# Kernel tuning notes

Hardware: AMD Instinct MI355X
Metric: run time of the kernel (lower is better)

## Reference

```python
import jax, jax.numpy as jnp
import numpy as np

B, N, C, H = 2048, 15, 1024, 16
HS = C // H  # 64
SCALE = HS ** -0.5
EPS = 1e-5


def _ln(x, g, b):
    m = jnp.mean(x, axis=-1, keepdims=True)
    v = jnp.mean(jnp.square(x - m), axis=-1, keepdims=True)
    return (x - m) * jax.lax.rsqrt(v + EPS) * g + b


def setup_inputs() -> dict:
    key = jax.random.key(0)
    ks = jax.random.split(key, 20)
    s = lambda fan_in: 1.0 / np.sqrt(fan_in)
    inp = {
        "joint_feature": jax.random.normal(ks[0], (B, N, C), jnp.float32),
        "relation_feature": jax.random.normal(ks[1], (B, N, C), jnp.float32),
        # weights stored as [in, out] (transposed vs torch Linear)
        "W_Jqkv": jax.random.uniform(ks[2], (C, 3 * C), jnp.float32, -s(C), s(C)),
        "W_Iqk": jax.random.uniform(ks[3], (C, 3 * C), jnp.float32, -s(C), s(C)),
        "W_Iconv": jax.random.uniform(ks[4], (HS, 15), jnp.float32, -s(HS), s(HS)),
        "W_proj": jax.random.uniform(ks[5], (C, C), jnp.float32, -s(C), s(C)),
        "b_proj": jax.random.uniform(ks[6], (C,), jnp.float32, -s(C), s(C)),
        "g_attn1": jnp.ones((C,), jnp.float32),
        "b_attn1": jnp.zeros((C,), jnp.float32),
        "g_attn2": jnp.ones((C,), jnp.float32),
        "b_attn2": jnp.zeros((C,), jnp.float32),
        "g_joint": jnp.ones((C,), jnp.float32),
        "b_joint": jnp.zeros((C,), jnp.float32),
        "W_fc1": jax.random.uniform(ks[7], (C, C // 2), jnp.float32, -s(C), s(C)),
        "b_fc1": jax.random.uniform(ks[8], (C // 2,), jnp.float32, -s(C), s(C)),
        "W_fc2": jax.random.uniform(ks[9], (C // 2, C), jnp.float32, -s(C // 2), s(C // 2)),
        "b_fc2": jax.random.uniform(ks[10], (C,), jnp.float32, -s(C // 2), s(C // 2)),
    }
    return inp


def reference(joint_feature, relation_feature, W_Jqkv, W_Iqk, W_Iconv, W_proj, b_proj,
              g_attn1, b_attn1, g_attn2, b_attn2, g_joint, b_joint,
              W_fc1, b_fc1, W_fc2, b_fc2):
    # --- Attention_I on normalized streams ---
    xj = _ln(joint_feature, g_attn1, b_attn1)      # [B,N,C]
    xi = _ln(relation_feature, g_attn2, b_attn2)   # [B,N,C]

    Jqkv = (xj @ W_Jqkv).reshape(B, N, 3, H, HS).transpose(2, 0, 3, 1, 4)  # [3,B,H,N,HS]
    Jq, Jk, Jv = Jqkv[0], Jqkv[1], Jqkv[2]
    Iqkv = (xi @ W_Iqk).reshape(B, N, 3, H, HS).transpose(2, 0, 3, 1, 4)
    Iq, Ik, Iv = Iqkv[0], Iqkv[1], Iqkv[2]

    attn_J = jnp.einsum("bhqd,bhkd->bhqk", Jq, Jk)
    attn_I = jnp.einsum("bhqd,bhkd->bhqk", Iq, Ik)
    attn_lin = Iv @ W_Iconv                        # [B,H,N,15] == [B,H,N,N]
    attn = jax.nn.softmax((attn_J + attn_I + attn_lin) * SCALE, axis=-1)

    x = jnp.einsum("bhqk,bhkd->bhqd", attn, Jv)    # [B,H,N,HS]
    x = x.transpose(0, 2, 1, 3).reshape(B, N, C)
    x = x @ W_proj + b_proj

    joint = joint_feature + x

    # --- MLP (hidden = dim // 2) ---
    y = _ln(joint, g_joint, b_joint)
    y = jax.nn.gelu(y @ W_fc1 + b_fc1, approximate=False)
    y = y @ W_fc2 + b_fc2
    return joint + y
```

## Files before the change

### kernel.cpp

```cpp
#include <hip/hip_runtime.h>
#include <math.h>


typedef __attribute__((ext_vector_type(8))) short short8;
typedef __attribute__((ext_vector_type(8))) unsigned short ush8;
typedef __attribute__((ext_vector_type(4))) float fx4;

#define MROWS 30720

#define GLL16(g, l)                                                         \
    __builtin_amdgcn_global_load_lds(                                       \
        (const __attribute__((address_space(1))) unsigned int*)(g),         \
        (__attribute__((address_space(3))) unsigned int*)(l), 16, 0, 0)

__device__ inline unsigned short f2bf(float f) {
    unsigned int u = __float_as_uint(f);
    unsigned int r = (u + 0x7fffu + ((u >> 16) & 1u)) >> 16;
    return (unsigned short)r;
}
__device__ inline float bf2f(unsigned short s) {
    return __uint_as_float(((unsigned int)s) << 16);
}

__global__ __launch_bounds__(256) void transpose_w(const float* __restrict__ W,
                                                   unsigned short* __restrict__ Wt,
                                                   int K, int N) {
    __shared__ float tile[32][33];
    int bn = blockIdx.x * 32;
    int bk = blockIdx.y * 32;
    int tx = threadIdx.x & 31, ty = threadIdx.x >> 5;
    #pragma unroll
    for (int i = ty; i < 32; i += 8)
        tile[i][tx] = W[(size_t)(bk + i) * N + bn + tx];
    __syncthreads();
    #pragma unroll
    for (int i = ty; i < 32; i += 8)
        Wt[(size_t)(bn + i) * K + bk + tx] = f2bf(tile[tx][i]);
}

__global__ __launch_bounds__(256) void ln_dual(const float* __restrict__ xa,
                                               const float* __restrict__ ga,
                                               const float* __restrict__ bba,
                                               unsigned short* __restrict__ oa,
                                               const float* __restrict__ xb,
                                               const float* __restrict__ gb,
                                               const float* __restrict__ bbb,
                                               unsigned short* __restrict__ ob) {
    const float* x = blockIdx.y ? xb : xa;
    const float* g = blockIdx.y ? gb : ga;
    const float* bv = blockIdx.y ? bbb : bba;
    unsigned short* out = blockIdx.y ? ob : oa;

    int row = blockIdx.x;
    int t = threadIdx.x;
    const float4* xp = (const float4*)(x + (size_t)row * 1024);
    float4 v = xp[t];
    float s  = v.x + v.y + v.z + v.w;
    float ss = v.x * v.x + v.y * v.y + v.z * v.z + v.w * v.w;
    #pragma unroll
    for (int o = 32; o > 0; o >>= 1) { s += __shfl_down(s, o); ss += __shfl_down(ss, o); }
    __shared__ float ps[4], pss[4], stat[2];
    int wv = t >> 6, ln = t & 63;
    if (ln == 0) { ps[wv] = s; pss[wv] = ss; }
    __syncthreads();
    if (t == 0) {
        float S = ps[0] + ps[1] + ps[2] + ps[3];
        float SS = pss[0] + pss[1] + pss[2] + pss[3];
        float m = S * (1.0f / 1024.0f);
        float var = SS * (1.0f / 1024.0f) - m * m;
        stat[0] = m; stat[1] = rsqrtf(var + 1e-5f);
    }
    __syncthreads();
    float m = stat[0], r = stat[1];
    float4 gg = ((const float4*)g)[t];
    float4 bb = ((const float4*)bv)[t];
    ushort4 o;
    o.x = f2bf((v.x - m) * r * gg.x + bb.x);
    o.y = f2bf((v.y - m) * r * gg.y + bb.y);
    o.z = f2bf((v.z - m) * r * gg.z + bb.z);
    o.w = f2bf((v.w - m) * r * gg.w + bb.w);
    ((ushort4*)(out + (size_t)row * 1024))[t] = o;
}

template <int EPI, int K>
__global__ __launch_bounds__(256) void gemm_lds(const unsigned short* __restrict__ A,
                                                const unsigned short* __restrict__ Bt,
                                                const unsigned short* __restrict__ A2,
                                                const unsigned short* __restrict__ Bt2,
                                                const float* __restrict__ bias,
                                                const float* __restrict__ resid,
                                                float* __restrict__ outF,
                                                unsigned short* __restrict__ outB,
                                                unsigned short* __restrict__ outB2,
                                                int N) {
    if (EPI == 0 && blockIdx.z) { A = A2; Bt = Bt2; outB = outB2; }

    __shared__ __align__(16) char smem[32768];
    unsigned short* lA = (unsigned short*)smem;
    unsigned short* lB = (unsigned short*)(smem + 16384);

    const int tid = threadIdx.x;
    const int wave = tid >> 6, lane = tid & 63;
    const int rowf = lane & 15, quad = lane >> 4;

    int bx = blockIdx.x, by = blockIdx.y;
    if (gridDim.x <= 8) {
        int nwg = gridDim.x * gridDim.y;
        int lid = by * gridDim.x + bx;
        int q = nwg >> 3, r = nwg & 7;
        int xcd = lid & 7, pos = lid >> 3;
        int nl = (xcd < r ? xcd * (q + 1) : r * (q + 1) + (xcd - r) * q) + pos;
        bx = nl % gridDim.x;
        by = nl / gridDim.x;
    }

    const int m0 = by * 128;
    const int n0 = bx * 128;
    const int wm0 = (wave >> 1) * 64;
    const int wn0 = (wave & 1) * 64;

    const int srow = tid >> 2;
    const int skc  = (tid & 3) * 8;
    const unsigned short* gA0 = A  + (size_t)(m0 + srow) * K + skc;
    const unsigned short* gA1 = A  + (size_t)(m0 + srow + 64) * K + skc;
    const unsigned short* gB0 = Bt + (size_t)(n0 + srow) * K + skc;
    const unsigned short* gB1 = Bt + (size_t)(n0 + srow + 64) * K + skc;

    fx4 acc[4][4] = {};

    const int NT = K / 32;

    GLL16(gA0, lA + (size_t)tid * 8);
    GLL16(gA1, lA + (size_t)(tid + 256) * 8);
    GLL16(gB0, lB + (size_t)tid * 8);
    GLL16(gB1, lB + (size_t)(tid + 256) * 8);
    gA0 += 32; gA1 += 32; gB0 += 32; gB1 += 32;
    __syncthreads();

    #pragma unroll 2
    for (int t = 0; t < NT; ++t) {
        const int cur = t & 1, nxt = cur ^ 1;
        if (t + 1 < NT) {
            GLL16(gA0, lA + nxt * 4096 + (size_t)tid * 8);
            GLL16(gA1, lA + nxt * 4096 + (size_t)(tid + 256) * 8);
            GLL16(gB0, lB + nxt * 4096 + (size_t)tid * 8);
            GLL16(gB1, lB + nxt * 4096 + (size_t)(tid + 256) * 8);
            gA0 += 32; gA1 += 32; gB0 += 32; gB1 += 32;
        }
        const unsigned short* sA = lA + cur * 4096;
        const unsigned short* sB = lB + cur * 4096;
        short8 a[4], b[4];
        #pragma unroll
        for (int i = 0; i < 4; i++)
            a[i] = *(const short8*)(sA + (wm0 + 16 * i + rowf) * 32 + quad * 8);
        #pragma unroll
        for (int j = 0; j < 4; j++)
            b[j] = *(const short8*)(sB + (wn0 + 16 * j + rowf) * 32 + quad * 8);
        #pragma unroll
        for (int i = 0; i < 4; i++)
            #pragma unroll
            for (int j = 0; j < 4; j++)
                acc[i][j] = __builtin_amdgcn_mfma_f32_16x16x32_bf16(a[i], b[j], acc[i][j], 0, 0, 0);
        asm volatile("s_waitcnt vmcnt(0) lgkmcnt(0)\n\ts_barrier" ::: "memory");
    }

    float* st = (float*)smem + wave * 1280;
    const int rl  = lane >> 2;
    const int c0l = (lane & 3) * 16;
    const int colb = n0 + wn0 + c0l;

    #pragma unroll
    for (int i = 0; i < 4; i++) {
        #pragma unroll
        for (int j = 0; j < 4; j++)
            #pragma unroll
            for (int r = 0; r < 4; r++)
                st[(quad * 4 + r) * 80 + 16 * j + rowf] = acc[i][j][r];
        const int row = m0 + wm0 + 16 * i + rl;
        if (EPI == 1) {
            #pragma unroll
            for (int kk = 0; kk < 4; kk++) {
                float4 v  = *(const float4*)(st + rl * 80 + c0l + 4 * kk);
                float4 bb = *((const float4*)(bias + colb) + kk);
                float4 rr = *((const float4*)(resid + (size_t)row * N + colb) + kk);
                v.x += bb.x + rr.x; v.y += bb.y + rr.y;
                v.z += bb.z + rr.z; v.w += bb.w + rr.w;
                *((float4*)(outF + (size_t)row * N + colb) + kk) = v;
            }
        } else {
            #pragma unroll
            for (int h = 0; h < 2; h++) {
                float4 va = *(const float4*)(st + rl * 80 + c0l + 8 * h);
                float4 vb = *(const float4*)(st + rl * 80 + c0l + 8 * h + 4);
                float f[8] = {va.x, va.y, va.z, va.w, vb.x, vb.y, vb.z, vb.w};
                if (EPI == 2) {
                    float4 ba = *((const float4*)(bias + colb) + 2 * h);
                    float4 bc = *((const float4*)(bias + colb) + 2 * h + 1);
                    float bf[8] = {ba.x, ba.y, ba.z, ba.w, bc.x, bc.y, bc.z, bc.w};
                    #pragma unroll
                    for (int e = 0; e < 8; e++) {
                        float v = f[e] + bf[e];
                        f[e] = 0.5f * v * (1.0f + erff(v * 0.70710678118654752f));
                    }
                }
                ush8 o;
                #pragma unroll
                for (int e = 0; e < 8; e++) o[e] = f2bf(f[e]);
                *(ush8*)(outB + (size_t)row * N + colb + 8 * h) = o;
            }
        }
    }
}

__global__ __launch_bounds__(256) void attn_kernel(const unsigned short* __restrict__ Jqkv,
                                                   const unsigned short* __restrict__ Iqkv,
                                                   const float* __restrict__ Wc,
                                                   unsigned short* __restrict__ xout) {
    int b = blockIdx.x >> 4;
    int h = blockIdx.x & 15;
    __shared__ float J[3][15][65];
    __shared__ float I[3][15][65];
    __shared__ float W[64][17];
    __shared__ float P[15][16];

    const unsigned short* Jb = Jqkv + (size_t)b * 15 * 3072 + h * 64;
    const unsigned short* Ib = Iqkv + (size_t)b * 15 * 3072 + h * 64;

    for (int idx = threadIdx.x; idx < 360; idx += 256) {
        int n = idx / 24, rem = idx % 24;
        int r = rem >> 3, d0 = (rem & 7) * 8;
        short8 vj = *(const short8*)(Jb + (size_t)n * 3072 + r * 1024 + d0);
        short8 vi = *(const short8*)(Ib + (size_t)n * 3072 + r * 1024 + d0);
        #pragma unroll
        for (int e = 0; e < 8; e++) {
            J[r][n][d0 + e] = bf2f((unsigned short)vj[e]);
            I[r][n][d0 + e] = bf2f((unsigned short)vi[e]);
        }
    }
    for (int idx = threadIdx.x; idx < 64 * 15; idx += 256)
        W[idx / 15][idx % 15] = Wc[idx];
    __syncthreads();

    for (int idx = threadIdx.x; idx < 225; idx += 256) {
        int q = idx / 15, kk = idx % 15;
        float s = 0.0f;
        #pragma unroll 8
        for (int d = 0; d < 64; d++)
            s += J[0][q][d] * J[1][kk][d] + I[0][q][d] * I[1][kk][d] + I[2][q][d] * W[d][kk];
        P[q][kk] = s * 0.125f;
    }
    __syncthreads();

    if (threadIdx.x < 15) {
        int q = threadIdx.x;
        float mx = -1e30f;
        #pragma unroll
        for (int kk = 0; kk < 15; kk++) mx = fmaxf(mx, P[q][kk]);
        float e[15], sum = 0.0f;
        #pragma unroll
        for (int kk = 0; kk < 15; kk++) { e[kk] = __expf(P[q][kk] - mx); sum += e[kk]; }
        float inv = 1.0f / sum;
        #pragma unroll
        for (int kk = 0; kk < 15; kk++) P[q][kk] = e[kk] * inv;
    }
    __syncthreads();

    for (int idx = threadIdx.x; idx < 240; idx += 256) {
        int q = idx >> 4, d0 = (idx & 15) * 4;
        float o0 = 0.0f, o1 = 0.0f, o2 = 0.0f, o3 = 0.0f;
        #pragma unroll
        for (int kk = 0; kk < 15; kk++) {
            float p = P[q][kk];
            o0 += p * J[2][kk][d0 + 0];
            o1 += p * J[2][kk][d0 + 1];
            o2 += p * J[2][kk][d0 + 2];
            o3 += p * J[2][kk][d0 + 3];
        }
        ushort4 o;
        o.x = f2bf(o0); o.y = f2bf(o1); o.z = f2bf(o2); o.w = f2bf(o3);
        *(ushort4*)(xout + ((size_t)b * 15 + q) * 1024 + h * 64 + d0) = o;
    }
}

extern "C" void kernel_launch(void* const* d_in, const int* in_sizes, int n_in,
                              void* d_out, int out_size, void* d_ws, size_t ws_size,
                              hipStream_t stream) {
    const float* joint_feature    = (const float*)d_in[0];
    const float* relation_feature = (const float*)d_in[1];
    const float* W_Jqkv  = (const float*)d_in[2];
    const float* W_Iqk   = (const float*)d_in[3];
    const float* W_Iconv = (const float*)d_in[4];
    const float* W_proj  = (const float*)d_in[5];
    const float* b_proj  = (const float*)d_in[6];
    const float* g1  = (const float*)d_in[7];
    const float* be1 = (const float*)d_in[8];
    const float* g2  = (const float*)d_in[9];
    const float* be2 = (const float*)d_in[10];
    const float* gj  = (const float*)d_in[11];
    const float* bj  = (const float*)d_in[12];
    const float* W_fc1 = (const float*)d_in[13];
    const float* b_fc1 = (const float*)d_in[14];
    const float* W_fc2 = (const float*)d_in[15];
    const float* b_fc2 = (const float*)d_in[16];

    char* ws = (char*)d_ws;
    unsigned short* WtJ  = (unsigned short*)(ws + 0);
    unsigned short* WtI  = (unsigned short*)(ws + 6291456);
    unsigned short* WtP  = (unsigned short*)(ws + 12582912);
    unsigned short* WtF1 = (unsigned short*)(ws + 14680064);
    unsigned short* WtF2 = (unsigned short*)(ws + 15728640);
    unsigned short* xj   = (unsigned short*)(ws + 16777216);
    unsigned short* xi   = (unsigned short*)(ws + 79691776);
    unsigned short* xattn = (unsigned short*)(ws + 142606336);
    float*          joint = (float*)(ws + 16777216);
    unsigned short* yln   = xattn;
    unsigned short* h1    = (unsigned short*)(ws + 205520896);
    int CH = 16;
    {
        const int opts[5] = {1, 2, 4, 8, 16};
        for (int i = 0; i < 5; i++) {
            size_t need = 205520896ull + 754974720ull / (size_t)opts[i];
            if (need <= ws_size) { CH = opts[i]; break; }
        }
    }
    const int Mc = MROWS / CH;
    const size_t chunkBytes = 754974720ull / (size_t)CH / 2ull;
    unsigned short* Jqkv_c = (unsigned short*)(ws + 205520896);
    unsigned short* Iqkv_c = (unsigned short*)(ws + 205520896 + chunkBytes);

    dim3 blk(256);

    transpose_w<<<dim3(96, 32), blk, 0, stream>>>(W_Jqkv, WtJ, 1024, 3072);
    transpose_w<<<dim3(96, 32), blk, 0, stream>>>(W_Iqk,  WtI, 1024, 3072);
    transpose_w<<<dim3(32, 32), blk, 0, stream>>>(W_proj, WtP, 1024, 1024);
    transpose_w<<<dim3(16, 32), blk, 0, stream>>>(W_fc1, WtF1, 1024, 512);
    transpose_w<<<dim3(32, 16), blk, 0, stream>>>(W_fc2, WtF2, 512, 1024);

    ln_dual<<<dim3(MROWS, 2), blk, 0, stream>>>(joint_feature, g1, be1, xj,
                                                relation_feature, g2, be2, xi);

    for (int c = 0; c < CH; c++) {
        size_t ro = (size_t)c * Mc * 1024;
        gemm_lds<0, 1024><<<dim3(24, Mc / 128, 2), blk, 0, stream>>>(
            xj + ro, WtJ, xi + ro, WtI, nullptr, nullptr, nullptr, Jqkv_c, Iqkv_c, 3072);
        attn_kernel<<<(Mc / 15) * 16, blk, 0, stream>>>(Jqkv_c, Iqkv_c, W_Iconv, xattn + ro);
    }

    gemm_lds<1, 1024><<<dim3(8, 240), blk, 0, stream>>>(
        xattn, WtP, nullptr, nullptr, b_proj, joint_feature, joint, nullptr, nullptr, 1024);

    ln_dual<<<dim3(MROWS, 1), blk, 0, stream>>>(joint, gj, bj, yln,
                                                nullptr, nullptr, nullptr, nullptr);

    gemm_lds<2, 1024><<<dim3(4, 240), blk, 0, stream>>>(
        yln, WtF1, nullptr, nullptr, b_fc1, nullptr, nullptr, h1, nullptr, 512);

    gemm_lds<1, 512><<<dim3(8, 240), blk, 0, stream>>>(
        h1, WtF2, nullptr, nullptr, b_fc2, joint, (float*)d_out, nullptr, nullptr, 1024);
}
```

Before: 1.456 ms.

## Triple-buffer GEMM LDS pipeline with partial vmcnt waits and MFMA priority

The GEMM main loop moves from double to triple buffering of the A/B tiles in LDS. Loads are issued two stages ahead, and each step waits only until the oldest stage has landed (vmcnt 8/4/0) instead of draining all loads every iteration. MFMA sections are wrapped in s_setprio, and the epilogue staging stride is padded from 80 to 84 floats to reduce LDS bank conflicts. LDS use grows from 32KB to 48KB per block, which may reduce occupancy, and each iteration now has two barriers.

Measured after the change: 1.442 ms. No clear change (-1.0%).

```diff
diff --git a/kernel.cpp b/kernel.cpp
--- a/kernel.cpp
+++ b/kernel.cpp
@@ -95,9 +95,9 @@
                                                 int N) {
     if (EPI == 0 && blockIdx.z) { A = A2; Bt = Bt2; outB = outB2; }
 
-    __shared__ __align__(16) char smem[32768];
+    __shared__ __align__(16) char smem[49152];
     unsigned short* lA = (unsigned short*)smem;
-    unsigned short* lB = (unsigned short*)(smem + 16384);
+    unsigned short* lB = (unsigned short*)(smem + 24576);
 
     const int tid = threadIdx.x;
     const int wave = tid >> 6, lane = tid & 63;
@@ -126,45 +126,57 @@
     const unsigned short* gB0 = Bt + (size_t)(n0 + srow) * K + skc;
     const unsigned short* gB1 = Bt + (size_t)(n0 + srow + 64) * K + skc;
 
+#define STAGE(pa, pb)                                                       \
+    do {                                                                    \
+        GLL16(gA0, (pa) + (size_t)tid * 8);                                 \
+        GLL16(gA1, (pa) + (size_t)(tid + 256) * 8);                         \
+        GLL16(gB0, (pb) + (size_t)tid * 8);                                 \
+        GLL16(gB1, (pb) + (size_t)(tid + 256) * 8);                         \
+        gA0 += 32; gA1 += 32; gB0 += 32; gB1 += 32;                         \
+    } while (0)
+
     fx4 acc[4][4] = {};
-
     const int NT = K / 32;
 
-    GLL16(gA0, lA + (size_t)tid * 8);
-    GLL16(gA1, lA + (size_t)(tid + 256) * 8);
-    GLL16(gB0, lB + (size_t)tid * 8);
-    GLL16(gB1, lB + (size_t)(tid + 256) * 8);
-    gA0 += 32; gA1 += 32; gB0 += 32; gB1 += 32;
-    __syncthreads();
-
-    #pragma unroll 2
+    unsigned short *pa0 = lA, *pa1 = lA + 4096, *pa2 = lA + 8192;
+    unsigned short *pb0 = lB, *pb1 = lB + 4096, *pb2 = lB + 8192;
+
+    STAGE(pa0, pb0);
+    STAGE(pa1, pb1);
+
     for (int t = 0; t < NT; ++t) {
-        const int cur = t & 1, nxt = cur ^ 1;
-        if (t + 1 < NT) {
-            GLL16(gA0, lA + nxt * 4096 + (size_t)tid * 8);
-            GLL16(gA1, lA + nxt * 4096 + (size_t)(tid + 256) * 8);
-            GLL16(gB0, lB + nxt * 4096 + (size_t)tid * 8);
-            GLL16(gB1, lB + nxt * 4096 + (size_t)(tid + 256) * 8);
-            gA0 += 32; gA1 += 32; gB0 += 32; gB1 += 32;
-        }
-        const unsigned short* sA = lA + cur * 4096;
-        const unsigned short* sB = lB + cur * 4096;
+        if (t + 2 < NT) {
+            STAGE(pa2, pb2);
+            asm volatile("s_waitcnt vmcnt(8)" ::: "memory");
+        } else if (t + 1 < NT) {
+            asm volatile("s_waitcnt vmcnt(4)" ::: "memory");
+        } else {
+            asm volatile("s_waitcnt vmcnt(0)" ::: "memory");
+        }
+        asm volatile("s_barrier" ::: "memory");
+
         short8 a[4], b[4];
         #pragma unroll
         for (int i = 0; i < 4; i++)
-            a[i] = *(const short8*)(sA + (wm0 + 16 * i + rowf) * 32 + quad * 8);
+            a[i] = *(const short8*)(pa0 + (wm0 + 16 * i + rowf) * 32 + quad * 8);
         #pragma unroll
         for (int j = 0; j < 4; j++)
-            b[j] = *(const short8*)(sB + (wn0 + 16 * j + rowf) * 32 + quad * 8);
+            b[j] = *(const short8*)(pb0 + (wn0 + 16 * j + rowf) * 32 + quad * 8);
+        __builtin_amdgcn_s_setprio(1);
         #pragma unroll
         for (int i = 0; i < 4; i++)
             #pragma unroll
             for (int j = 0; j < 4; j++)
                 acc[i][j] = __builtin_amdgcn_mfma_f32_16x16x32_bf16(a[i], b[j], acc[i][j], 0, 0, 0);
-        asm volatile("s_waitcnt vmcnt(0) lgkmcnt(0)\n\ts_barrier" ::: "memory");
-    }
-
-    float* st = (float*)smem + wave * 1280;
+        __builtin_amdgcn_s_setprio(0);
+        asm volatile("s_barrier" ::: "memory");
+
+        unsigned short* ta = pa0; pa0 = pa1; pa1 = pa2; pa2 = ta;
+        unsigned short* tb = pb0; pb0 = pb1; pb1 = pb2; pb2 = tb;
+    }
+#undef STAGE
+
+    float* st = (float*)smem + wave * 1344;
     const int rl  = lane >> 2;
     const int c0l = (lane & 3) * 16;
     const int colb = n0 + wn0 + c0l;
@@ -175,12 +187,12 @@
         for (int j = 0; j < 4; j++)
             #pragma unroll
             for (int r = 0; r < 4; r++)
-                st[(quad * 4 + r) * 80 + 16 * j + rowf] = acc[i][j][r];
+                st[(quad * 4 + r) * 84 + 16 * j + rowf] = acc[i][j][r];
         const int row = m0 + wm0 + 16 * i + rl;
         if (EPI == 1) {
             #pragma unroll
             for (int kk = 0; kk < 4; kk++) {
-                float4 v  = *(const float4*)(st + rl * 80 + c0l + 4 * kk);
+                float4 v  = *(const float4*)(st + rl * 84 + c0l + 4 * kk);
                 float4 bb = *((const float4*)(bias + colb) + kk);
                 float4 rr = *((const float4*)(resid + (size_t)row * N + colb) + kk);
                 v.x += bb.x + rr.x; v.y += bb.y + rr.y;
@@ -190,8 +202,8 @@
         } else {
             #pragma unroll
             for (int h = 0; h < 2; h++) {
-                float4 va = *(const float4*)(st + rl * 80 + c0l + 8 * h);
-                float4 vb = *(const float4*)(st + rl * 80 + c0l + 8 * h + 4);
+                float4 va = *(const float4*)(st + rl * 84 + c0l + 8 * h);
+                float4 vb = *(const float4*)(st + rl * 84 + c0l + 8 * h + 4);
                 float f[8] = {va.x, va.y, va.z, va.w, vb.x, vb.y, vb.z, vb.w};
                 if (EPI == 2) {
                     float4 ba = *((const float4*)(bias + colb) + 2 * h);
```

## Replace 128x128 GEMM with 256x256-tile, 512-thread, swizzled-LDS pipelined GEMM

Applied to the files above, without the earlier changes.

Replaces the 128x128, 256-thread bf16 MFMA GEMM with a 256x256 tile on 8 waves and a K-step of 64. LDS holds 128KB double-buffered, with XOR-swizzled columns to avoid bank conflicts. Global-to-LDS staging is interleaved in quarter-steps between MFMA groups, with s_setprio and partial vmcnt waits. The aim is more operand reuse per byte loaded and better overlap of loads with matrix math. The cost is fewer workgroups (e.g. 2x120 for fc1), which risks underfilling the CUs, plus a row bound check for chunks that are not multiples of 256.

After: 1.368 ms. 1.06x faster.

```diff
diff --git a/kernel.cpp b/kernel.cpp
--- a/kernel.cpp
+++ b/kernel.cpp
@@ -3,7 +3,6 @@
 
 
 typedef __attribute__((ext_vector_type(8))) short short8;
-typedef __attribute__((ext_vector_type(8))) unsigned short ush8;
 typedef __attribute__((ext_vector_type(4))) float fx4;
 
 #define MROWS 30720
@@ -83,28 +82,27 @@
 }
 
 template <int EPI, int K>
-__global__ __launch_bounds__(256) void gemm_lds(const unsigned short* __restrict__ A,
-                                                const unsigned short* __restrict__ Bt,
-                                                const unsigned short* __restrict__ A2,
-                                                const unsigned short* __restrict__ Bt2,
-                                                const float* __restrict__ bias,
-                                                const float* __restrict__ resid,
-                                                float* __restrict__ outF,
-                                                unsigned short* __restrict__ outB,
-                                                unsigned short* __restrict__ outB2,
-                                                int N) {
+__global__ __launch_bounds__(512, 2) void gemm256(const unsigned short* __restrict__ A,
+                                                  const unsigned short* __restrict__ Bt,
+                                                  const unsigned short* __restrict__ A2,
+                                                  const unsigned short* __restrict__ Bt2,
+                                                  const float* __restrict__ bias,
+                                                  const float* __restrict__ resid,
+                                                  float* __restrict__ outF,
+                                                  unsigned short* __restrict__ outB,
+                                                  unsigned short* __restrict__ outB2,
+                                                  int N, int Mtot) {
     if (EPI == 0 && blockIdx.z) { A = A2; Bt = Bt2; outB = outB2; }
 
-    __shared__ __align__(16) char smem[32768];
-    unsigned short* lA = (unsigned short*)smem;
-    unsigned short* lB = (unsigned short*)(smem + 16384);
+    __shared__ unsigned short sm[65536];
 
     const int tid = threadIdx.x;
-    const int wave = tid >> 6, lane = tid & 63;
+    const int wid = tid >> 6, lane = tid & 63;
     const int rowf = lane & 15, quad = lane >> 4;
+    const int wrow = wid >> 2, wcol = wid & 3;
 
     int bx = blockIdx.x, by = blockIdx.y;
-    if (gridDim.x <= 8) {
+    {
         int nwg = gridDim.x * gridDim.y;
         int lid = by * gridDim.x + bx;
         int q = nwg >> 3, r = nwg & 7;
@@ -113,100 +111,154 @@
         bx = nl % gridDim.x;
         by = nl / gridDim.x;
     }
-
-    const int m0 = by * 128;
-    const int n0 = bx * 128;
-    const int wm0 = (wave >> 1) * 64;
-    const int wn0 = (wave & 1) * 64;
-
-    const int srow = tid >> 2;
-    const int skc  = (tid & 3) * 8;
-    const unsigned short* gA0 = A  + (size_t)(m0 + srow) * K + skc;
-    const unsigned short* gA1 = A  + (size_t)(m0 + srow + 64) * K + skc;
-    const unsigned short* gB0 = Bt + (size_t)(n0 + srow) * K + skc;
-    const unsigned short* gB1 = Bt + (size_t)(n0 + srow + 64) * K + skc;
-
-    fx4 acc[4][4] = {};
-
-    const int NT = K / 32;
-
-    GLL16(gA0, lA + (size_t)tid * 8);
-    GLL16(gA1, lA + (size_t)(tid + 256) * 8);
-    GLL16(gB0, lB + (size_t)tid * 8);
-    GLL16(gB1, lB + (size_t)(tid + 256) * 8);
-    gA0 += 32; gA1 += 32; gB0 += 32; gB1 += 32;
-    __syncthreads();
+    const int m0 = by * 256, n0 = bx * 256;
+
+    const int srw  = tid >> 3;
+    const int scol = ((tid & 7) ^ (srw & 7)) << 3;
+    const unsigned short* pA[2][2];
+    const unsigned short* pB[2][2];
+    #pragma unroll
+    for (int h = 0; h < 2; h++)
+        #pragma unroll
+        for (int i = 0; i < 2; i++) {
+            pA[h][i] = A  + (size_t)(m0 + h * 128 + i * 64 + srw) * K + scol;
+            pB[h][i] = Bt + (size_t)(n0 + h * 128 + i * 64 + srw) * K + scol;
+        }
+
+    const int axk0 = rowf * 64 + ((quad ^ (rowf & 7)) << 3);
+    const int axk1 = rowf * 64 + (((4 + quad) ^ (rowf & 7)) << 3);
+
+    fx4 acc[8][4] = {};
+    short8 a[4][2], b[4][2];
+    const int NT = K / 64;
+
+#define STG_A(H, D)                                                         \
+    do {                                                                    \
+        GLL16(pA[H][0], sm + ((D) << 15) + (H) * 8192 + wid * 512);         \
+        GLL16(pA[H][1], sm + ((D) << 15) + (H) * 8192 + 4096 + wid * 512);  \
+        pA[H][0] += 64; pA[H][1] += 64;                                     \
+    } while (0)
+#define STG_B(H, D)                                                         \
+    do {                                                                    \
+        GLL16(pB[H][0], sm + ((D) << 15) + 16384 + (H) * 8192 + wid * 512); \
+        GLL16(pB[H][1], sm + ((D) << 15) + 16384 + (H) * 8192 + 4096 + wid * 512); \
+        pB[H][0] += 64; pB[H][1] += 64;                                     \
+    } while (0)
+#define LDA4(BUFO, MS)                                                      \
+    do {                                                                    \
+        const unsigned short* _p = sm + (BUFO) + wrow * 8192 + (MS) * 4096; \
+        _Pragma("unroll") for (int mi = 0; mi < 4; mi++) {                  \
+            a[mi][0] = *(const short8*)(_p + mi * 1024 + axk0);             \
+            a[mi][1] = *(const short8*)(_p + mi * 1024 + axk1);             \
+        }                                                                   \
+    } while (0)
+#define LDB2(BUFO, PR)                                                      \
+    do {                                                                    \
+        const unsigned short* _p = sm + (BUFO) + 16384 + (wcol >> 1) * 8192 \
+                                   + (wcol & 1) * 4096 + (PR) * 2048;       \
+        _Pragma("unroll") for (int ni = 0; ni < 2; ni++) {                  \
+            b[(PR) * 2 + ni][0] = *(const short8*)(_p + ni * 1024 + axk0);  \
+            b[(PR) * 2 + ni][1] = *(const short8*)(_p + ni * 1024 + axk1);  \
+        }                                                                   \
+    } while (0)
+#define MM16(MS, PR)                                                        \
+    do {                                                                    \
+        __builtin_amdgcn_s_setprio(1);                                      \
+        _Pragma("unroll") for (int mi = 0; mi < 4; mi++)                    \
+        _Pragma("unroll") for (int ni = 0; ni < 2; ni++) {                  \
+            fx4 _c = acc[(MS) * 4 + mi][(PR) * 2 + ni];                     \
+            _c = __builtin_amdgcn_mfma_f32_16x16x32_bf16(a[mi][0], b[(PR) * 2 + ni][0], _c, 0, 0, 0); \
+            _c = __builtin_amdgcn_mfma_f32_16x16x32_bf16(a[mi][1], b[(PR) * 2 + ni][1], _c, 0, 0, 0); \
+            acc[(MS) * 4 + mi][(PR) * 2 + ni] = _c;                         \
+        }                                                                   \
+        __builtin_amdgcn_s_setprio(0);                                      \
+    } while (0)
+
+    STG_A(0, 0); STG_A(1, 0); STG_B(0, 0); STG_B(1, 0);
+    STG_B(0, 1);
+    STG_A(0, 1);
+    asm volatile("s_waitcnt vmcnt(4)" ::: "memory");
+    __builtin_amdgcn_s_barrier();
 
     #pragma unroll 2
     for (int t = 0; t < NT; ++t) {
-        const int cur = t & 1, nxt = cur ^ 1;
-        if (t + 1 < NT) {
-            GLL16(gA0, lA + nxt * 4096 + (size_t)tid * 8);
-            GLL16(gA1, lA + nxt * 4096 + (size_t)(tid + 256) * 8);
-            GLL16(gB0, lB + nxt * 4096 + (size_t)tid * 8);
-            GLL16(gB1, lB + nxt * 4096 + (size_t)(tid + 256) * 8);
-            gA0 += 32; gA1 += 32; gB0 += 32; gB1 += 32;
-        }
-        const unsigned short* sA = lA + cur * 4096;
-        const unsigned short* sB = lB + cur * 4096;
-        short8 a[4], b[4];
-        #pragma unroll
-        for (int i = 0; i < 4; i++)
-            a[i] = *(const short8*)(sA + (wm0 + 16 * i + rowf) * 32 + quad * 8);
-        #pragma unroll
-        for (int j = 0; j < 4; j++)
-            b[j] = *(const short8*)(sB + (wn0 + 16 * j + rowf) * 32 + quad * 8);
-        #pragma unroll
-        for (int i = 0; i < 4; i++)
-            #pragma unroll
-            for (int j = 0; j < 4; j++)
-                acc[i][j] = __builtin_amdgcn_mfma_f32_16x16x32_bf16(a[i], b[j], acc[i][j], 0, 0, 0);
-        asm volatile("s_waitcnt vmcnt(0) lgkmcnt(0)\n\ts_barrier" ::: "memory");
-    }
-
-    float* st = (float*)smem + wave * 1280;
-    const int rl  = lane >> 2;
-    const int c0l = (lane & 3) * 16;
-    const int colb = n0 + wn0 + c0l;
+        const int bufo = (t & 1) << 15;
+        const bool s1 = (t + 1 < NT);
+        const bool s2 = (t + 2 < NT);
+
+        if (s1) STG_A(1, (t + 1) & 1);
+        LDA4(bufo, 0);
+        LDB2(bufo, 0);
+        MM16(0, 0);
+
+        if (s1) STG_B(1, (t + 1) & 1);
+        LDB2(bufo, 1);
+        MM16(0, 1);
+        __builtin_amdgcn_sched_barrier(0);
+        __builtin_amdgcn_s_barrier();
+
+        if (s2) STG_B(0, t & 1);
+        LDA4(bufo, 1);
+        MM16(1, 1);
+        __builtin_amdgcn_sched_barrier(0);
+        __builtin_amdgcn_s_barrier();
+
+        if (s2) STG_A(0, t & 1);
+        MM16(1, 0);
+        if (s1) {
+            if (s2) asm volatile("s_waitcnt vmcnt(4)" ::: "memory");
+            else    asm volatile("s_waitcnt vmcnt(0)" ::: "memory");
+        }
+        __builtin_amdgcn_sched_barrier(0);
+        __builtin_amdgcn_s_barrier();
+    }
+#undef STG_A
+#undef STG_B
+#undef LDA4
+#undef LDB2
+#undef MM16
+
+    float* st = (float*)sm + wid * 1088;
+    const int c4 = lane & 15;
+    const int rquad = lane >> 4;
+    const int colb = n0 + wcol * 64 + c4 * 4;
+    float4 bb4 = {0.0f, 0.0f, 0.0f, 0.0f};
+    if (EPI != 0) bb4 = *(const float4*)(bias + colb);
 
     #pragma unroll
-    for (int i = 0; i < 4; i++) {
-        #pragma unroll
-        for (int j = 0; j < 4; j++)
+    for (int mf = 0; mf < 8; mf++) {
+        #pragma unroll
+        for (int nf = 0; nf < 4; nf++)
             #pragma unroll
             for (int r = 0; r < 4; r++)
-                st[(quad * 4 + r) * 80 + 16 * j + rowf] = acc[i][j][r];
-        const int row = m0 + wm0 + 16 * i + rl;
-        if (EPI == 1) {
-            #pragma unroll
-            for (int kk = 0; kk < 4; kk++) {
-                float4 v  = *(const float4*)(st + rl * 80 + c0l + 4 * kk);
-                float4 bb = *((const float4*)(bias + colb) + kk);
-                float4 rr = *((const float4*)(resid + (size_t)row * N + colb) + kk);
-                v.x += bb.x + rr.x; v.y += bb.y + rr.y;
-                v.z += bb.z + rr.z; v.w += bb.w + rr.w;
-                *((float4*)(outF + (size_t)row * N + colb) + kk) = v;
-            }
-        } else {
-            #pragma unroll
-            for (int h = 0; h < 2; h++) {
-                float4 va = *(const float4*)(st + rl * 80 + c0l + 8 * h);
-                float4 vb = *(const float4*)(st + rl * 80 + c0l + 8 * h + 4);
-                float f[8] = {va.x, va.y, va.z, va.w, vb.x, vb.y, vb.z, vb.w};
-                if (EPI == 2) {
-                    float4 ba = *((const float4*)(bias + colb) + 2 * h);
-                    float4 bc = *((const float4*)(bias + colb) + 2 * h + 1);
-                    float bf[8] = {ba.x, ba.y, ba.z, ba.w, bc.x, bc.y, bc.z, bc.w};
-                    #pragma unroll
-                    for (int e = 0; e < 8; e++) {
-                        float v = f[e] + bf[e];
-                        f[e] = 0.5f * v * (1.0f + erff(v * 0.70710678118654752f));
-                    }
+                st[(quad * 4 + r) * 68 + nf * 16 + rowf] = acc[mf][nf][r];
+        #pragma unroll
+        for (int rr = 0; rr < 4; rr++) {
+            int lrow = rr * 4 + rquad;
+            float4 v = *(const float4*)(st + lrow * 68 + c4 * 4);
+            int grow = m0 + wrow * 128 + mf * 16 + lrow;
+            if (grow < Mtot) {
+                size_t off = (size_t)grow * N + colb;
+                if (EPI == 1) {
+                    float4 rr4 = *(const float4*)(resid + off);
+                    v.x += bb4.x + rr4.x; v.y += bb4.y + rr4.y;
+                    v.z += bb4.z + rr4.z; v.w += bb4.w + rr4.w;
+                    *(float4*)(outF + off) = v;
+                } else if (EPI == 2) {
+                    float f0 = v.x + bb4.x, f1 = v.y + bb4.y;
+                    float f2 = v.z + bb4.z, f3 = v.w + bb4.w;
+                    f0 = 0.5f * f0 * (1.0f + erff(f0 * 0.70710678118654752f));
+                    f1 = 0.5f * f1 * (1.0f + erff(f1 * 0.70710678118654752f));
+                    f2 = 0.5f * f2 * (1.0f + erff(f2 * 0.70710678118654752f));
+                    f3 = 0.5f * f3 * (1.0f + erff(f3 * 0.70710678118654752f));
+                    ushort4 o;
+                    o.x = f2bf(f0); o.y = f2bf(f1); o.z = f2bf(f2); o.w = f2bf(f3);
+                    *(ushort4*)(outB + off) = o;
+                } else {
+                    ushort4 o;
+                    o.x = f2bf(v.x); o.y = f2bf(v.y); o.z = f2bf(v.z); o.w = f2bf(v.w);
+                    *(ushort4*)(outB + off) = o;
                 }
-                ush8 o;
-                #pragma unroll
-                for (int e = 0; e < 8; e++) o[e] = f2bf(f[e]);
-                *(ush8*)(outB + (size_t)row * N + colb + 8 * h) = o;
             }
         }
     }
@@ -329,6 +381,7 @@
     unsigned short* Iqkv_c = (unsigned short*)(ws + 205520896 + chunkBytes);
 
     dim3 blk(256);
+    dim3 blk5(512);
 
     transpose_w<<<dim3(96, 32), blk, 0, stream>>>(W_Jqkv, WtJ, 1024, 3072);
     transpose_w<<<dim3(96, 32), blk, 0, stream>>>(W_Iqk,  WtI, 1024, 3072);
@@ -339,22 +392,23 @@
     ln_dual<<<dim3(MROWS, 2), blk, 0, stream>>>(joint_feature, g1, be1, xj,
                                                 relation_feature, g2, be2, xi);
 
+    const int My = (Mc + 255) >> 8;
     for (int c = 0; c < CH; c++) {
         size_t ro = (size_t)c * Mc * 1024;
-        gemm_lds<0, 1024><<<dim3(24, Mc / 128, 2), blk, 0, stream>>>(
-            xj + ro, WtJ, xi + ro, WtI, nullptr, nullptr, nullptr, Jqkv_c, Iqkv_c, 3072);
+        gemm256<0, 1024><<<dim3(12, My, 2), blk5, 0, stream>>>(
+            xj + ro, WtJ, xi + ro, WtI, nullptr, nullptr, nullptr, Jqkv_c, Iqkv_c, 3072, Mc);
         attn_kernel<<<(Mc / 15) * 16, blk, 0, stream>>>(Jqkv_c, Iqkv_c, W_Iconv, xattn + ro);
     }
 
-    gemm_lds<1, 1024><<<dim3(8, 240), blk, 0, stream>>>(
-        xattn, WtP, nullptr, nullptr, b_proj, joint_feature, joint, nullptr, nullptr, 1024);
+    gemm256<1, 1024><<<dim3(4, 120), blk5, 0, stream>>>(
+        xattn, WtP, nullptr, nullptr, b_proj, joint_feature, joint, nullptr, nullptr, 1024, MROWS);
 
     ln_dual<<<dim3(MROWS, 1), blk, 0, stream>>>(joint, gj, bj, yln,
                                                 nullptr, nullptr, nullptr, nullptr);
 
-    gemm_lds<2, 1024><<<dim3(4, 240), blk, 0, stream>>>(
-        yln, WtF1, nullptr, nullptr, b_fc1, nullptr, nullptr, h1, nullptr, 512);
-
-    gemm_lds<1, 512><<<dim3(8, 240), blk, 0, stream>>>(
-        h1, WtF2, nullptr, nullptr, b_fc2, joint, (float*)d_out, nullptr, nullptr, 1024);
-}
+    gemm256<2, 1024><<<dim3(2, 120), blk5, 0, stream>>>(
+        yln, WtF1, nullptr, nullptr, b_fc1, nullptr, nullptr, h1, nullptr, 512, MROWS);
+
+    gemm256<1, 512><<<dim3(4, 120), blk5, 0, stream>>>(
+        h1, WtF2, nullptr, nullptr, b_fc2, joint, (float*)d_out, nullptr, nullptr, 1024, MROWS);
+}
```
